# Kernel optimization log

Hardware: AMD Instinct MI355X
Metric: run time of the kernel (lower is better)

The kernel has to match this reference:

```python
import jax, jax.numpy as jnp
import numpy as np

D = 512; H = 8; HD = D // H; L = 6; QD = 16; MAXLEN = 1000

def _pos_encoding(max_len, d):
    pos = jnp.arange(max_len, dtype=jnp.float32)[:, None]
    div = jnp.exp(jnp.arange(0, d, 2, dtype=jnp.float32) * (-np.log(10000.0) / d))
    pe = jnp.zeros((max_len, d), jnp.float32)
    pe = pe.at[:, 0::2].set(jnp.sin(pos * div))
    pe = pe.at[:, 1::2].set(jnp.cos(pos * div))
    return pe

def _quantum(x, W, b, qwr, qwi, sg, em, mb):
    # QuantumInspiredLayer: classical tanh branch + quantum branch fused by sigmoid gate
    classical = jnp.tanh(x @ W + b)
    qs = x @ sg                          # (B,S,QD) real superposition amplitudes
    ev_r = qs @ qwr                      # complex evolution, real/imag parts kept separate
    ev_i = qs @ qwi
    en_r = ev_r @ em                     # entanglement (real matrix)
    en_i = ev_i @ em
    probs = en_r ** 2 + en_i ** 2        # |entangled|^2, (B,S,QD)
    qout = probs @ mb                    # measurement, (B,S,D)
    fw = jax.nn.sigmoid(jnp.mean(probs, axis=-1, keepdims=True))  # (B,S,1)
    return fw * qout + (1.0 - fw) * classical, probs

def _layer(x, p):
    (Wq, bq, Wk, bk, Wv, bv, Wo, bo,
     qW, qb, qr, qi, qsg, qem, qmb,
     kW, kb, kr, ki, ksg, kem, kmb, g, beta) = p
    B, S, _ = x.shape
    Q = x @ Wq + bq
    K = x @ Wk + bk
    Vv = x @ Wv + bv
    Qq, qp = _quantum(x, qW, qb, qr, qi, qsg, qem, qmb)
    Kq, kp = _quantum(x, kW, kb, kr, ki, ksg, kem, kmb)
    Qf = (0.7 * Q + 0.3 * Qq).reshape(B, S, H, HD).transpose(0, 2, 1, 3)  # (B,H,S,hd)
    Kf = (0.7 * K + 0.3 * Kq).reshape(B, S, H, HD).transpose(0, 2, 1, 3)
    Vh = Vv.reshape(B, S, H, HD).transpose(0, 2, 1, 3)
    scores = jnp.einsum('bhid,bhjd->bhij', Qf, Kf) / np.sqrt(HD).astype(np.float32)
    interf = jnp.einsum('biq,bjq->bij', qp, kp)   # quantum interference term (B,S,S)
    scores = scores + 0.1 * interf[:, None]       # broadcast over heads
    attn = jax.nn.softmax(scores, axis=-1)        # dropout=eval mode (identity)
    ctx = jnp.einsum('bhij,bhjd->bhid', attn, Vh).transpose(0, 2, 1, 3).reshape(B, S, D)
    y = ctx @ Wo + bo + x                         # residual, then LayerNorm
    mu = jnp.mean(y, axis=-1, keepdims=True)
    var = jnp.mean((y - mu) ** 2, axis=-1, keepdims=True)
    y = (y - mu) / jnp.sqrt(var + 1e-5) * g + beta
    return y, attn

def setup_inputs() -> dict:
    key = jax.random.key(0)
    ks = iter(jax.random.split(key, 64))
    def rn(shape, s=0.02):
        return (jax.random.normal(next(ks), shape) * s).astype(jnp.float32)
    B, S, V = 4, 512, 32000
    inp = {
        'text_input': jax.random.randint(next(ks), (B, S), 0, V),
        'visual_input': rn((B, 2048), 1.0),
        'temporal_input': rn((B, 64), 1.0),
        'embed': rn((V, D)),
        'Wvis': rn((2048, D)), 'bvis': jnp.zeros((D,), jnp.float32),
        'Wtemp': rn((64, D)), 'btemp': jnp.zeros((D,), jnp.float32),
        'Wq': rn((L, D, D)), 'bq': jnp.zeros((L, D), jnp.float32),
        'Wk': rn((L, D, D)), 'bk': jnp.zeros((L, D), jnp.float32),
        'Wv': rn((L, D, D)), 'bv': jnp.zeros((L, D), jnp.float32),
        'Wo': rn((L, D, D)), 'bo': jnp.zeros((L, D), jnp.float32),
        'qW': rn((L, D, D)), 'qb': jnp.zeros((L, D), jnp.float32),
        'q_qwr': rn((L, QD, QD), 0.05), 'q_qwi': rn((L, QD, QD), 0.05),
        'q_sg': rn((L, D, QD), 0.05), 'q_em': rn((L, QD, QD), 0.05), 'q_mb': rn((L, QD, D), 0.05),
        'kW': rn((L, D, D)), 'kb': jnp.zeros((L, D), jnp.float32),
        'k_qwr': rn((L, QD, QD), 0.05), 'k_qwi': rn((L, QD, QD), 0.05),
        'k_sg': rn((L, D, QD), 0.05), 'k_em': rn((L, QD, QD), 0.05), 'k_mb': rn((L, QD, D), 0.05),
        'ln_g': jnp.ones((L, D), jnp.float32), 'ln_b': jnp.zeros((L, D), jnp.float32),
        'Ws': rn((D, 64)), 'bs_': jnp.zeros((64,), jnp.float32),
        'Wd': rn((D, 5)), 'bd': jnp.zeros((5,), jnp.float32),
        'We': rn((D, 1)), 'be': jnp.zeros((1,), jnp.float32),
    }
    return inp

def reference(text_input, visual_input, temporal_input, embed, Wvis, bvis, Wtemp, btemp,
              Wq, bq, Wk, bk, Wv, bv, Wo, bo,
              qW, qb, q_qwr, q_qwi, q_sg, q_em, q_mb,
              kW, kb, k_qwr, k_qwi, k_sg, k_em, k_mb,
              ln_g, ln_b, Ws, bs_, Wd, bd, We, be):
    B, S = text_input.shape
    x = (embed[text_input]
         + (visual_input @ Wvis + bvis)[:, None, :]
         + (temporal_input @ Wtemp + btemp)[:, None, :])
    x = x + _pos_encoding(MAXLEN, D)[None, :S, :]
    attns = []
    for l in range(L):
        p = (Wq[l], bq[l], Wk[l], bk[l], Wv[l], bv[l], Wo[l], bo[l],
             qW[l], qb[l], q_qwr[l], q_qwi[l], q_sg[l], q_em[l], q_mb[l],
             kW[l], kb[l], k_qwr[l], k_qwi[l], k_sg[l], k_em[l], k_mb[l],
             ln_g[l], ln_b[l])
        x, a = _layer(x, p)
        attns.append(a)
    pooled = jnp.mean(x, axis=1)  # no attention_mask -> simple mean pool
    skill = jax.nn.sigmoid(pooled @ Ws + bs_)
    diff = jax.nn.softmax(pooled @ Wd + bd, axis=-1)
    eng = jax.nn.sigmoid(pooled @ We + be)
    return skill, diff, eng, x, jnp.stack(attns)
```

## Files before the change

### kernel.cpp

```cpp
#include <hip/hip_runtime.h>
#include <hip/hip_bf16.h>

typedef __attribute__((ext_vector_type(4))) float f32x4;
typedef __attribute__((ext_vector_type(8))) short s16x8;

__device__ __forceinline__ unsigned short f2b(float f) {
  unsigned int u = __float_as_uint(f);
  unsigned int r = (u + 0x7FFFu + ((u >> 16) & 1u)) >> 16;
  return (unsigned short)r;
}
__device__ __forceinline__ float b2f(unsigned short h) {
  return __uint_as_float(((unsigned int)h) << 16);
}
__device__ __forceinline__ void gload16(const void* g, void* l) {
  __builtin_amdgcn_global_load_lds(
      (const __attribute__((address_space(1))) void*)g,
      (__attribute__((address_space(3))) void*)l, 16, 0, 0);
}

enum { MODE_F32 = 0, MODE_VT = 1, MODE_Y = 2 };
struct OutSpec { void* ptr; int mode; };
struct Outs5 { OutSpec o[5]; };
struct Ptr6 { const float* p[6]; };

template<int BM, int BN, int WGM, int WGN>
__global__ __launch_bounds__(256) void gemm_nt(
    const unsigned short* __restrict__ A, int lda, long long strideA,
    const unsigned short* __restrict__ Bm, int ldb, long long strideB,
    const float* __restrict__ biasBase, int biasStride, int perZ,
    Outs5 outs, const float* __restrict__ resid, int K)
{
  constexpr int BK = 32;
  constexpr int WM = BM / WGM, WN = BN / WGN;
  constexpr int WR = WM / 16, WC = WN / 16;
  constexpr int CHA = BM * BK / 8;
  constexpr int CHB = BN * BK / 8;
  __shared__ unsigned short lds_a[2][BM * BK];
  __shared__ unsigned short lds_b[2][BN * BK];
  const int z = blockIdx.z;
  const int tid = threadIdx.x;
  const int wave = tid >> 6, lane = tid & 63;
  const int l16 = lane & 15, lhi = lane >> 4;
  const int wm = (wave / WGN) * WM, wn = (wave % WGN) * WN;
  const int m0 = blockIdx.x * BM, n0 = blockIdx.y * BN;
  const unsigned short* Ap = A + (long long)z * strideA;
  const unsigned short* Bp = Bm + (long long)z * strideB;

  auto stage = [&](int buf, int k0) {
#pragma unroll
    for (int p = 0; p < CHA / 256; ++p) {
      int t = p * 256 + tid;
      gload16(Ap + (long long)(m0 + (t >> 2)) * lda + k0 + (t & 3) * 8, &lds_a[buf][t * 8]);
    }
    if constexpr (CHA % 256) {
      if (tid < CHA % 256) {
        int t = (CHA / 256) * 256 + tid;
        gload16(Ap + (long long)(m0 + (t >> 2)) * lda + k0 + (t & 3) * 8, &lds_a[buf][t * 8]);
      }
    }
#pragma unroll
    for (int p = 0; p < CHB / 256; ++p) {
      int t = p * 256 + tid;
      gload16(Bp + (long long)(n0 + (t >> 2)) * ldb + k0 + (t & 3) * 8, &lds_b[buf][t * 8]);
    }
    if constexpr (CHB % 256) {
      if (tid < CHB % 256) {
        int t = (CHB / 256) * 256 + tid;
        gload16(Bp + (long long)(n0 + (t >> 2)) * ldb + k0 + (t & 3) * 8, &lds_b[buf][t * 8]);
      }
    }
  };

  f32x4 acc[WR][WC];
#pragma unroll
  for (int r = 0; r < WR; ++r)
#pragma unroll
    for (int c = 0; c < WC; ++c) { f32x4 zz = {0.f, 0.f, 0.f, 0.f}; acc[r][c] = zz; }

  stage(0, 0);
  __syncthreads();
  int cur = 0;
  for (int k0 = 0; k0 < K; k0 += BK) {
    if (k0 + BK < K) stage(cur ^ 1, k0 + BK);
    s16x8 af[WR], bfv[WC];
#pragma unroll
    for (int r = 0; r < WR; ++r)
      af[r] = *(const s16x8*)&lds_a[cur][(wm + r * 16 + l16) * BK + lhi * 8];
#pragma unroll
    for (int c = 0; c < WC; ++c)
      bfv[c] = *(const s16x8*)&lds_b[cur][(wn + c * 16 + l16) * BK + lhi * 8];
#pragma unroll
    for (int r = 0; r < WR; ++r)
#pragma unroll
      for (int c = 0; c < WC; ++c)
        acc[r][c] = __builtin_amdgcn_mfma_f32_16x16x32_bf16(af[r], bfv[c], acc[r][c], 0, 0, 0);
    __syncthreads();
    cur ^= 1;
  }

  OutSpec spec = perZ ? outs.o[z] : outs.o[0];
  const float* bias = biasBase ? (biasBase + (long long)z * biasStride) : nullptr;
#pragma unroll
  for (int r = 0; r < WR; ++r) {
#pragma unroll
    for (int c = 0; c < WC; ++c) {
      int n = n0 + wn + c * 16 + l16;
      int rb = m0 + wm + r * 16 + lhi * 4;
      float bv = bias ? bias[n] : 0.f;
      float vv[4];
#pragma unroll
      for (int j = 0; j < 4; ++j) vv[j] = acc[r][c][j] + bv;
      if (spec.mode == MODE_F32) {
#pragma unroll
        for (int j = 0; j < 4; ++j)
          ((float*)spec.ptr)[(long long)(rb + j) * 512 + n] = vv[j];
      } else if (spec.mode == MODE_VT) {
        int b = rb >> 9, s = rb & 511;
        ushort4 pk;
        pk.x = f2b(vv[0]); pk.y = f2b(vv[1]); pk.z = f2b(vv[2]); pk.w = f2b(vv[3]);
        *(ushort4*)&((unsigned short*)spec.ptr)[
            (((long long)(b * 8 + (n >> 6))) * 64 + (n & 63)) * 512 + s] = pk;
      } else {
#pragma unroll
        for (int j = 0; j < 4; ++j)
          ((float*)spec.ptr)[(long long)(rb + j) * 512 + n] =
              vv[j] + resid[(long long)(rb + j) * 512 + n];
      }
    }
  }
}

__global__ __launch_bounds__(256, 1) void fused_attn(
    const unsigned short* __restrict__ Qe, const unsigned short* __restrict__ Ke,
    const unsigned short* __restrict__ Vt, float* __restrict__ attn,
    unsigned short* __restrict__ ctx)
{
  __shared__ unsigned short lds[55296];
  const int z = blockIdx.x, rb = blockIdx.y;
  const int m0 = rb * 64;
  const int b = z >> 3, h = z & 7;
  const int tid = threadIdx.x;
  const int w = tid >> 6, lane = tid & 63;
  const int l16 = lane & 15, lhi = lane >> 4;
  const int rx3 = l16 & 3, rx7 = l16 & 7;

#pragma unroll
  for (int p = 0; p < 3; ++p) {
    int t = p * 256 + tid;
    int row = t / 12, c = t % 12;
    gload16(Qe + ((long long)(z * 512 + m0 + row)) * 96 + (c ^ (row & 3)) * 8, &lds[t * 8]);
  }
#pragma unroll
  for (int p = 0; p < 24; ++p) {
    int t = p * 256 + tid;
    int row = t / 12, c = t % 12;
    gload16(Ke + ((long long)(z * 512 + row)) * 96 + (c ^ (row & 3)) * 8, &lds[6144 + t * 8]);
  }
  __syncthreads();

  const unsigned short* Qs = lds;
  const unsigned short* Ks = lds + 6144;
  s16x8 aq[3];
#pragma unroll
  for (int kk = 0; kk < 3; ++kk)
    aq[kk] = *(const s16x8*)&Qs[(w * 16 + l16) * 96 + (kk * 4 + (lhi ^ rx3)) * 8];
  f32x4 acc[32];
#pragma unroll
  for (int c = 0; c < 32; ++c) { f32x4 zz = {0.f, 0.f, 0.f, 0.f}; acc[c] = zz; }
#pragma unroll
  for (int c = 0; c < 32; ++c) {
#pragma unroll
    for (int kk = 0; kk < 3; ++kk) {
      s16x8 bf = *(const s16x8*)&Ks[(c * 16 + l16) * 96 + (kk * 4 + (lhi ^ rx3)) * 8];
      acc[c] = __builtin_amdgcn_mfma_f32_16x16x32_bf16(aq[kk], bf, acc[c], 0, 0, 0);
    }
  }

  float inv[4];
#pragma unroll
  for (int j = 0; j < 4; ++j) {
    float mx = acc[0][j];
#pragma unroll
    for (int c = 1; c < 32; ++c) mx = fmaxf(mx, acc[c][j]);
    mx = fmaxf(mx, __shfl_xor(mx, 1));
    mx = fmaxf(mx, __shfl_xor(mx, 2));
    mx = fmaxf(mx, __shfl_xor(mx, 4));
    mx = fmaxf(mx, __shfl_xor(mx, 8));
    float sum = 0.f;
#pragma unroll
    for (int c = 0; c < 32; ++c) { float e = __expf(acc[c][j] - mx); acc[c][j] = e; sum += e; }
    sum += __shfl_xor(sum, 1);
    sum += __shfl_xor(sum, 2);
    sum += __shfl_xor(sum, 4);
    sum += __shfl_xor(sum, 8);
    inv[j] = 1.f / sum;
  }
  __syncthreads();

#pragma unroll
  for (int p = 0; p < 8; ++p) {
    int t = p * 256 + tid;
    int row = t >> 5, c = t & 31;
    gload16(Vt + (long long)z * 32768 + row * 512 + (c ^ (row & 7)) * 8, &lds[32768 + t * 8]);
  }
  unsigned short* S = lds;
  {
    float* ap = attn + (long long)z * 262144;
#pragma unroll
    for (int j = 0; j < 4; ++j) {
      int row_l = w * 16 + lhi * 4 + j;
      int rs = row_l & 7;
      float* arow = ap + (long long)(m0 + row_l) * 512;
      unsigned short* srow = S + row_l * 512;
#pragma unroll
      for (int c = 0; c < 32; ++c) {
        float p = acc[c][j] * inv[j];
        int col = c * 16 + l16;
        arow[col] = p;
        srow[((col >> 3) ^ rs) * 8 + (col & 7)] = f2b(p);
      }
    }
  }
  __syncthreads();

  const unsigned short* Vl = lds + 32768;
  f32x4 acc2[4];
#pragma unroll
  for (int c2 = 0; c2 < 4; ++c2) { f32x4 zz = {0.f, 0.f, 0.f, 0.f}; acc2[c2] = zz; }
  const int qrow = w * 16 + l16;
#pragma unroll
  for (int kk = 0; kk < 8; ++kk) {
    s16x8 a = *(const s16x8*)&S[qrow * 512 + ((kk * 4 + lhi) ^ rx7) * 8];
#pragma unroll
    for (int c2 = 0; c2 < 4; ++c2) {
      s16x8 bf = *(const s16x8*)&Vl[(c2 * 16 + l16) * 256 + ((kk * 4 + lhi) ^ rx7) * 8];
      acc2[c2] = __builtin_amdgcn_mfma_f32_16x16x32_bf16(a, bf, acc2[c2], 0, 0, 0);
    }
  }
  __syncthreads();
#pragma unroll
  for (int p = 0; p < 8; ++p) {
    int t = p * 256 + tid;
    int row = t >> 5, c = t & 31;
    gload16(Vt + (long long)z * 32768 + row * 512 + 256 + (c ^ (row & 7)) * 8,
            &lds[32768 + t * 8]);
  }
  __syncthreads();
#pragma unroll
  for (int kk = 8; kk < 16; ++kk) {
    s16x8 a = *(const s16x8*)&S[qrow * 512 + ((kk * 4 + lhi) ^ rx7) * 8];
#pragma unroll
    for (int c2 = 0; c2 < 4; ++c2) {
      s16x8 bf = *(const s16x8*)&Vl[(c2 * 16 + l16) * 256 + (((kk - 8) * 4 + lhi) ^ rx7) * 8];
      acc2[c2] = __builtin_amdgcn_mfma_f32_16x16x32_bf16(a, bf, acc2[c2], 0, 0, 0);
    }
  }
#pragma unroll
  for (int c2 = 0; c2 < 4; ++c2) {
#pragma unroll
    for (int j = 0; j < 4; ++j) {
      int row_g = m0 + w * 16 + lhi * 4 + j;
      ctx[((long long)(b * 512 + row_g)) * 512 + h * 64 + c2 * 16 + l16] = f2b(acc2[c2][j]);
    }
  }
}

__global__ __launch_bounds__(256) void wt_k(Ptr6 srcs, unsigned short* __restrict__ wt) {
  __shared__ float tile[32][33];
  int zz = blockIdx.z;
  int l = zz / 6, mat = zz % 6;
  const float* src = srcs.p[mat] + (long long)l * 262144;
  int tx = threadIdx.x, ty = threadIdx.y;
  int n0 = blockIdx.x * 32, k0 = blockIdx.y * 32;
#pragma unroll
  for (int r = 0; r < 4; ++r)
    tile[ty + r * 8][tx] = src[(long long)(k0 + ty + r * 8) * 512 + n0 + tx];
  __syncthreads();
#pragma unroll
  for (int r = 0; r < 4; ++r)
    wt[(long long)zz * 262144 + (long long)(n0 + ty + r * 8) * 512 + k0 + tx] =
        f2b(tile[tx][ty + r * 8]);
}

__global__ __launch_bounds__(256) void prep_k(Ptr6 biases,
    const float* __restrict__ qwr, const float* __restrict__ qwi, const float* __restrict__ qem,
    const float* __restrict__ kwr, const float* __restrict__ kwi, const float* __restrict__ kem,
    float* __restrict__ biasPacked, float* __restrict__ ArAi) {
  int l = blockIdx.x, t = threadIdx.x;
  for (int m = 0; m < 6; ++m)
    for (int d = t; d < 512; d += 256)
      biasPacked[(l * 6 + m) * 512 + d] = biases.p[m][l * 512 + d];
  int i = t >> 4, j = t & 15;
  const float* em0 = qem + l * 256;
  float ar = 0.f, ai = 0.f;
  for (int tt = 0; tt < 16; ++tt) {
    ar += qwr[l * 256 + i * 16 + tt] * em0[tt * 16 + j];
    ai += qwi[l * 256 + i * 16 + tt] * em0[tt * 16 + j];
  }
  ArAi[(l * 4 + 0) * 256 + t] = ar;
  ArAi[(l * 4 + 1) * 256 + t] = ai;
  const float* em1 = kem + l * 256;
  ar = 0.f; ai = 0.f;
  for (int tt = 0; tt < 16; ++tt) {
    ar += kwr[l * 256 + i * 16 + tt] * em1[tt * 16 + j];
    ai += kwi[l * 256 + i * 16 + tt] * em1[tt * 16 + j];
  }
  ArAi[(l * 4 + 2) * 256 + t] = ar;
  ArAi[(l * 4 + 3) * 256 + t] = ai;
}

__global__ __launch_bounds__(512) void vispart_k(const float* __restrict__ vis,
    const float* __restrict__ Wvis, float* __restrict__ part) {
  int b = blockIdx.x, chunk = blockIdx.y, d = threadIdx.x;
  float acc = 0.f;
  for (int k = chunk * 64; k < chunk * 64 + 64; ++k)
    acc += vis[b * 2048 + k] * Wvis[(long long)k * 512 + d];
  part[(b * 32 + chunk) * 512 + d] = acc;
}
__global__ __launch_bounds__(512) void projsum_k(const float* __restrict__ part,
    const float* __restrict__ bvis, const float* __restrict__ temporal,
    const float* __restrict__ Wtemp, const float* __restrict__ btemp, float* __restrict__ proj) {
  int b = blockIdx.x, d = threadIdx.x;
  float acc = bvis[d] + btemp[d];
  for (int c = 0; c < 32; ++c) acc += part[(b * 32 + c) * 512 + d];
  for (int k = 0; k < 64; ++k) acc += temporal[b * 64 + k] * Wtemp[k * 512 + d];
  proj[b * 512 + d] = acc;
}

__global__ __launch_bounds__(512) void embed_k(const int* __restrict__ text,
    const float* __restrict__ emb, const float* __restrict__ proj,
    float* __restrict__ x, unsigned short* __restrict__ xb) {
  int row = blockIdx.x;
  int b = row >> 9, s = row & 511;
  int d = threadIdx.x;
  int tok = text[row];
  float v = emb[(long long)tok * 512 + d] + proj[b * 512 + d];
  float fr = __expf((float)((d >> 1) << 1) * (-9.2103403719761836f / 512.f));
  float ang = (float)s * fr;
  v += (d & 1) ? cosf(ang) : sinf(ang);
  x[(long long)row * 512 + d] = v;
  xb[(long long)row * 512 + d] = f2b(v);
}

__global__ __launch_bounds__(64) void quantum_k(const float* __restrict__ x,
    const float* __restrict__ sg_q, const float* __restrict__ sg_k,
    const float* __restrict__ ArAiL, float* __restrict__ qp, float* __restrict__ kp,
    float* __restrict__ fwq, float* __restrict__ fwk) {
  int row = blockIdx.x, side = blockIdx.y, lane = threadIdx.x;
  const float* sg = side ? sg_k : sg_q;
  const float* Ar = ArAiL + side * 512;
  const float* Ai = Ar + 256;
  float acc[16];
#pragma unroll
  for (int j = 0; j < 16; ++j) acc[j] = 0.f;
  const float* xr = x + (long long)row * 512;
#pragma unroll
  for (int kk = 0; kk < 8; ++kk) {
    float xv = xr[kk * 64 + lane];
    const float* sgr = sg + (kk * 64 + lane) * 16;
#pragma unroll
    for (int j = 0; j < 16; ++j) acc[j] += xv * sgr[j];
  }
#pragma unroll
  for (int s = 32; s; s >>= 1)
#pragma unroll
    for (int j = 0; j < 16; ++j) acc[j] += __shfl_xor(acc[j], s);
  int j = lane & 15;
  float tr = 0.f, ti = 0.f;
#pragma unroll
  for (int t = 0; t < 16; ++t) {
    tr += acc[t] * Ar[t * 16 + j];
    ti += acc[t] * Ai[t * 16 + j];
  }
  float p = tr * tr + ti * ti;
  float ps = p;
#pragma unroll
  for (int s = 1; s < 16; s <<= 1) ps += __shfl_xor(ps, s);
  if (lane < 16) (side ? kp : qp)[row * 16 + lane] = p;
  if (lane == 0) (side ? fwk : fwq)[row] = 1.f / (1.f + __expf(-ps * (1.f / 16.f)));
}

struct FuseP {
  const float* lin; const float* cl; const float* qp; const float* fw;
  const float* mb; unsigned short* ext; float sA, sB;
};
struct Fuse2 { FuseP s[2]; };
__global__ __launch_bounds__(512) void fuse_k(Fuse2 fp) {
  FuseP P = fp.s[blockIdx.y];
  int row = blockIdx.x;
  int b = row >> 9, i = row & 511;
  int d = threadIdx.x;
  const float* qpr = P.qp + row * 16;
  float fwv = P.fw[row];
  float qout = 0.f;
#pragma unroll
  for (int t = 0; t < 16; ++t) qout += qpr[t] * P.mb[t * 512 + d];
  float qq = fwv * qout + (1.f - fwv) * tanhf(P.cl[(long long)row * 512 + d]);
  float val = (0.7f * P.lin[(long long)row * 512 + d] + 0.3f * qq) * P.sA;
  int h = d >> 6, dd = d & 63;
  P.ext[(((long long)(b * 8 + h)) * 512 + i) * 96 + dd] = f2b(val);
  if (d < 128) {
    int h2 = d >> 4, j = d & 15;
    P.ext[(((long long)(b * 8 + h2)) * 512 + i) * 96 + 64 + j] = f2b(P.sB * qpr[j]);
  } else if (d < 256) {
    int t2 = d - 128;
    int h2 = t2 >> 4, j = t2 & 15;
    P.ext[(((long long)(b * 8 + h2)) * 512 + i) * 96 + 80 + j] = 0;
  }
}

__global__ __launch_bounds__(256) void ln_k(const float* __restrict__ y,
    const float* __restrict__ g, const float* __restrict__ be,
    float* __restrict__ xo, unsigned short* __restrict__ xb, float* __restrict__ xo2) {
  int wv = threadIdx.x >> 6, lane = threadIdx.x & 63;
  long long row = (long long)blockIdx.x * 4 + wv;
  const float* yr = y + row * 512 + lane * 8;
  f32x4 a = *(const f32x4*)yr, b = *(const f32x4*)(yr + 4);
  float s = a[0] + a[1] + a[2] + a[3] + b[0] + b[1] + b[2] + b[3];
#pragma unroll
  for (int m = 32; m; m >>= 1) s += __shfl_xor(s, m);
  float mu = s * (1.f / 512.f);
  float d[8], vs = 0.f;
#pragma unroll
  for (int j = 0; j < 4; ++j) { d[j] = a[j] - mu; vs += d[j] * d[j]; }
#pragma unroll
  for (int j = 0; j < 4; ++j) { d[4 + j] = b[j] - mu; vs += d[4 + j] * d[4 + j]; }
#pragma unroll
  for (int m = 32; m; m >>= 1) vs += __shfl_xor(vs, m);
  float rstd = rsqrtf(vs * (1.f / 512.f) + 1e-5f);
  f32x4 g0 = *(const f32x4*)(g + lane * 8), g1 = *(const f32x4*)(g + lane * 8 + 4);
  f32x4 b0 = *(const f32x4*)(be + lane * 8), b1 = *(const f32x4*)(be + lane * 8 + 4);
  f32x4 o0, o1; s16x8 ob;
#pragma unroll
  for (int j = 0; j < 4; ++j) { o0[j] = d[j] * rstd * g0[j] + b0[j]; ob[j] = (short)f2b(o0[j]); }
#pragma unroll
  for (int j = 0; j < 4; ++j) { o1[j] = d[4 + j] * rstd * g1[j] + b1[j]; ob[4 + j] = (short)f2b(o1[j]); }
  float* xr = xo + row * 512 + lane * 8;
  *(f32x4*)xr = o0; *(f32x4*)(xr + 4) = o1;
  *(s16x8*)(xb + row * 512 + lane * 8) = ob;
  if (xo2) {
    float* x2 = xo2 + row * 512 + lane * 8;
    *(f32x4*)x2 = o0; *(f32x4*)(x2 + 4) = o1;
  }
}

__global__ __launch_bounds__(512) void poolpart_k(const float* __restrict__ x,
                                                   float* __restrict__ part) {
  int b = blockIdx.x, ch = blockIdx.y, d = threadIdx.x;
  float s = 0.f;
  for (int r = 0; r < 64; ++r) s += x[((long long)(b * 512 + ch * 64 + r)) * 512 + d];
  part[(b * 8 + ch) * 512 + d] = s;
}
__global__ __launch_bounds__(512) void head_k(const float* __restrict__ part,
    const float* __restrict__ Ws, const float* __restrict__ bs,
    const float* __restrict__ Wd, const float* __restrict__ bd,
    const float* __restrict__ We, const float* __restrict__ be, float* __restrict__ out) {
  __shared__ float pooled[512];
  __shared__ float dl[5];
  int b = blockIdx.x, d = threadIdx.x;
  float s = 0.f;
  for (int t = 0; t < 8; ++t) s += part[(b * 8 + t) * 512 + d];
  pooled[d] = s * (1.f / 512.f);
  __syncthreads();
  if (d < 64) {
    float a = bs[d];
    for (int t = 0; t < 512; ++t) a += pooled[t] * Ws[t * 64 + d];
    out[b * 64 + d] = 1.f / (1.f + __expf(-a));
  } else if (d < 69) {
    int j = d - 64;
    float a = bd[j];
    for (int t = 0; t < 512; ++t) a += pooled[t] * Wd[t * 5 + j];
    dl[j] = a;
  } else if (d == 69) {
    float a = be[0];
    for (int t = 0; t < 512; ++t) a += pooled[t] * We[t];
    out[276 + b] = 1.f / (1.f + __expf(-a));
  }
  __syncthreads();
  if (d < 5) {
    float mx = dl[0];
    for (int j = 1; j < 5; ++j) mx = fmaxf(mx, dl[j]);
    float sm = 0.f;
    for (int j = 0; j < 5; ++j) sm += __expf(dl[j] - mx);
    out[256 + b * 5 + d] = __expf(dl[d] - mx) / sm;
  }
}

extern "C" void kernel_launch(void* const* d_in, const int* in_sizes, int n_in,
                              void* d_out, int out_size, void* d_ws, size_t ws_size,
                              hipStream_t stream) {
  (void)in_sizes; (void)n_in; (void)out_size; (void)ws_size;
  const int*   text     = (const int*)  d_in[0];
  const float* visual   = (const float*)d_in[1];
  const float* temporal = (const float*)d_in[2];
  const float* embedw   = (const float*)d_in[3];
  const float* Wvis  = (const float*)d_in[4];  const float* bvis  = (const float*)d_in[5];
  const float* Wtemp = (const float*)d_in[6];  const float* btemp = (const float*)d_in[7];
  const float* Wq = (const float*)d_in[8];   const float* bq = (const float*)d_in[9];
  const float* Wk = (const float*)d_in[10];  const float* bk = (const float*)d_in[11];
  const float* Wv = (const float*)d_in[12];  const float* bv = (const float*)d_in[13];
  const float* Wo = (const float*)d_in[14];  const float* bo = (const float*)d_in[15];
  const float* qW = (const float*)d_in[16];  const float* qb = (const float*)d_in[17];
  const float* q_qwr = (const float*)d_in[18]; const float* q_qwi = (const float*)d_in[19];
  const float* q_sg  = (const float*)d_in[20]; const float* q_em  = (const float*)d_in[21];
  const float* q_mb  = (const float*)d_in[22];
  const float* kW = (const float*)d_in[23];  const float* kb = (const float*)d_in[24];
  const float* k_qwr = (const float*)d_in[25]; const float* k_qwi = (const float*)d_in[26];
  const float* k_sg  = (const float*)d_in[27]; const float* k_em  = (const float*)d_in[28];
  const float* k_mb  = (const float*)d_in[29];
  const float* ln_g = (const float*)d_in[30]; const float* ln_b = (const float*)d_in[31];
  const float* Ws = (const float*)d_in[32];  const float* bs_ = (const float*)d_in[33];
  const float* Wd = (const float*)d_in[34];  const float* bd = (const float*)d_in[35];
  const float* We = (const float*)d_in[36];  const float* be = (const float*)d_in[37];
  float* out = (float*)d_out;

  char* w = (char*)d_ws;
  auto alloc = [&](size_t bytes) {
    char* p = w;
    w += (bytes + 255) & ~(size_t)255;
    return p;
  };
  float* ws_x   = (float*)alloc(2048ll * 512 * 4);
  unsigned short* ws_xb = (unsigned short*)alloc(2048ll * 512 * 2);
  unsigned short* ws_Wt = (unsigned short*)alloc(36ll * 262144 * 2);
  float* ws_bias = (float*)alloc(6ll * 6 * 512 * 4);
  float* ws_ArAi = (float*)alloc(6ll * 1024 * 4);
  float* ws_proj = (float*)alloc(4ll * 512 * 4);
  float* ws_vp   = (float*)alloc(4ll * 32 * 512 * 4);
  float* ws_Q    = (float*)alloc(2048ll * 512 * 4);
  float* ws_K    = (float*)alloc(2048ll * 512 * 4);
  float* ws_Cq   = (float*)alloc(2048ll * 512 * 4);
  float* ws_Ck   = (float*)alloc(2048ll * 512 * 4);
  float* ws_qp   = (float*)alloc(2048ll * 16 * 4);
  float* ws_kp   = (float*)alloc(2048ll * 16 * 4);
  float* ws_fwq  = (float*)alloc(2048ll * 4);
  float* ws_fwk  = (float*)alloc(2048ll * 4);
  unsigned short* ws_Vt   = (unsigned short*)alloc(2048ll * 512 * 2);
  unsigned short* ws_Qext = (unsigned short*)alloc(4ll * 8 * 512 * 96 * 2);
  unsigned short* ws_Kext = (unsigned short*)alloc(4ll * 8 * 512 * 96 * 2);
  unsigned short* ws_ctx  = (unsigned short*)alloc(2048ll * 512 * 2);
  float* ws_y    = (float*)alloc(2048ll * 512 * 4);

  Ptr6 wsrc = {{Wq, Wk, Wv, qW, kW, Wo}};
  wt_k<<<dim3(16, 16, 36), dim3(32, 8), 0, stream>>>(wsrc, ws_Wt);
  Ptr6 bsrc = {{bq, bk, bv, qb, kb, bo}};
  prep_k<<<dim3(6), dim3(256), 0, stream>>>(bsrc, q_qwr, q_qwi, q_em, k_qwr, k_qwi, k_em,
                                            ws_bias, ws_ArAi);
  vispart_k<<<dim3(4, 32), dim3(512), 0, stream>>>(visual, Wvis, ws_vp);
  projsum_k<<<dim3(4), dim3(512), 0, stream>>>(ws_vp, bvis, temporal, Wtemp, btemp, ws_proj);
  embed_k<<<dim3(2048), dim3(512), 0, stream>>>(text, embedw, ws_proj, ws_x, ws_xb);

  const long long ATTN_OFF = 280ll + 1048576ll;
  for (int l = 0; l < 6; ++l) {
    const unsigned short* WtL = ws_Wt + (long long)l * 6 * 262144;
    const float* biasL = ws_bias + (long long)l * 6 * 512;

    Outs5 o5{};
    o5.o[0] = { ws_Q, MODE_F32 };  o5.o[1] = { ws_K, MODE_F32 };
    o5.o[2] = { ws_Vt, MODE_VT };  o5.o[3] = { ws_Cq, MODE_F32 };
    o5.o[4] = { ws_Ck, MODE_F32 };
    gemm_nt<128, 128, 2, 2><<<dim3(16, 4, 5), 256, 0, stream>>>(
        ws_xb, 512, 0ll, WtL, 512, 262144ll, biasL, 512, 1, o5, nullptr, 512);

    quantum_k<<<dim3(2048, 2), 64, 0, stream>>>(ws_x, q_sg + l * 8192, k_sg + l * 8192,
        ws_ArAi + l * 1024, ws_qp, ws_kp, ws_fwq, ws_fwk);

    Fuse2 f2{};
    f2.s[0] = { ws_Q, ws_Cq, ws_qp, ws_fwq, q_mb + l * 8192, ws_Qext, 0.125f, 0.1f };
    f2.s[1] = { ws_K, ws_Ck, ws_kp, ws_fwk, k_mb + l * 8192, ws_Kext, 1.0f, 1.0f };
    fuse_k<<<dim3(2048, 2), dim3(512), 0, stream>>>(f2);

    fused_attn<<<dim3(32, 8), 256, 0, stream>>>(
        ws_Qext, ws_Kext, ws_Vt, out + ATTN_OFF + (long long)l * 8388608, ws_ctx);

    Outs5 oy{};
    oy.o[0] = { ws_y, MODE_Y };
    gemm_nt<64, 64, 2, 2><<<dim3(32, 8, 1), 256, 0, stream>>>(
        ws_ctx, 512, 0ll, WtL + 5 * 262144, 512, 0ll, biasL + 5 * 512, 0, 0, oy, ws_x, 512);

    ln_k<<<dim3(512), dim3(256), 0, stream>>>(ws_y, ln_g + l * 512, ln_b + l * 512,
        ws_x, ws_xb, (l == 5) ? (out + 280) : nullptr);
  }

  poolpart_k<<<dim3(4, 8), dim3(512), 0, stream>>>(ws_x, ws_vp);
  head_k<<<dim3(4), dim3(512), 0, stream>>>(ws_vp, Ws, bs_, Wd, bd, We, be, out);
}
```

Before: 507.8 us.

## Store GEMM intermediates in bf16 and prefetch K/V earlier in attention

The projection and Wo GEMM outputs (Q, K, classical branches and the pre-LayerNorm sum) are now stored as bf16 instead of fp32, and fuse_k and ln_k read bf16. This halves their memory traffic. quantum_k now reads the bf16 copy of x instead of the fp32 one. In fused_attn, K is loaded in two halves and the first V half is prefetched up front into a larger LDS buffer, with partial vmcnt waits and s_setprio so the QK^T MFMAs overlap the loads. In exchange, bf16 rounding of the residual sum before LayerNorm and of the quantum input may reduce accuracy, and the larger LDS footprint limits occupancy.

```diff
diff --git a/kernel.cpp b/kernel.cpp
--- a/kernel.cpp
+++ b/kernel.cpp
@@ -18,7 +18,7 @@
       (__attribute__((address_space(3))) void*)l, 16, 0, 0);
 }
 
-enum { MODE_F32 = 0, MODE_VT = 1, MODE_Y = 2 };
+enum { MODE_BF16 = 0, MODE_VT = 1, MODE_Y = 2 };
 struct OutSpec { void* ptr; int mode; };
 struct Outs5 { OutSpec o[5]; };
 struct Ptr6 { const float* p[6]; };
@@ -110,10 +110,10 @@
       float vv[4];
 #pragma unroll
       for (int j = 0; j < 4; ++j) vv[j] = acc[r][c][j] + bv;
-      if (spec.mode == MODE_F32) {
+      if (spec.mode == MODE_BF16) {
 #pragma unroll
         for (int j = 0; j < 4; ++j)
-          ((float*)spec.ptr)[(long long)(rb + j) * 512 + n] = vv[j];
+          ((unsigned short*)spec.ptr)[(long long)(rb + j) * 512 + n] = f2b(vv[j]);
       } else if (spec.mode == MODE_VT) {
         int b = rb >> 9, s = rb & 511;
         ushort4 pk;
@@ -123,8 +123,8 @@
       } else {
 #pragma unroll
         for (int j = 0; j < 4; ++j)
-          ((float*)spec.ptr)[(long long)(rb + j) * 512 + n] =
-              vv[j] + resid[(long long)(rb + j) * 512 + n];
+          ((unsigned short*)spec.ptr)[(long long)(rb + j) * 512 + n] =
+              f2b(vv[j] + resid[(long long)(rb + j) * 512 + n]);
       }
     }
   }
@@ -135,46 +135,73 @@
     const unsigned short* __restrict__ Vt, float* __restrict__ attn,
     unsigned short* __restrict__ ctx)
 {
-  __shared__ unsigned short lds[55296];
+  __shared__ unsigned short lds[71680];
   const int z = blockIdx.x, rb = blockIdx.y;
-  const int m0 = rb * 64;
-  const int b = z >> 3, h = z & 7;
-  const int tid = threadIdx.x;
-  const int w = tid >> 6, lane = tid & 63;
+  const int m0 = rb * 64, b = z >> 3, h = z & 7;
+  const int tid = threadIdx.x, w = tid >> 6, lane = tid & 63;
   const int l16 = lane & 15, lhi = lane >> 4;
   const int rx3 = l16 & 3, rx7 = l16 & 7;
+  const long long zs = (long long)z * 512;
 
 #pragma unroll
   for (int p = 0; p < 3; ++p) {
     int t = p * 256 + tid;
     int row = t / 12, c = t % 12;
-    gload16(Qe + ((long long)(z * 512 + m0 + row)) * 96 + (c ^ (row & 3)) * 8, &lds[t * 8]);
-  }
-#pragma unroll
-  for (int p = 0; p < 24; ++p) {
+    gload16(Qe + (zs + m0 + row) * 96 + (c ^ (row & 3)) * 8, &lds[t * 8]);
+  }
+#pragma unroll
+  for (int p = 0; p < 12; ++p) {
     int t = p * 256 + tid;
     int row = t / 12, c = t % 12;
-    gload16(Ke + ((long long)(z * 512 + row)) * 96 + (c ^ (row & 3)) * 8, &lds[6144 + t * 8]);
-  }
-  __syncthreads();
-
-  const unsigned short* Qs = lds;
-  const unsigned short* Ks = lds + 6144;
+    gload16(Ke + (zs + row) * 96 + (c ^ (row & 3)) * 8, &lds[6144 + t * 8]);
+  }
+#pragma unroll
+  for (int p = 0; p < 12; ++p) {
+    int t = p * 256 + tid;
+    int row = t / 12, c = t % 12;
+    gload16(Ke + (zs + 256 + row) * 96 + (c ^ (row & 3)) * 8, &lds[30720 + t * 8]);
+  }
+#pragma unroll
+  for (int p = 0; p < 8; ++p) {
+    int t = p * 256 + tid;
+    int row = t >> 5, c = t & 31;
+    gload16(Vt + (long long)z * 32768 + row * 512 + (c ^ (row & 7)) * 8, &lds[55296 + t * 8]);
+  }
+  asm volatile("s_waitcnt vmcnt(20)" ::: "memory");
+  __builtin_amdgcn_s_barrier();
+  __builtin_amdgcn_sched_barrier(0);
+
   s16x8 aq[3];
 #pragma unroll
   for (int kk = 0; kk < 3; ++kk)
-    aq[kk] = *(const s16x8*)&Qs[(w * 16 + l16) * 96 + (kk * 4 + (lhi ^ rx3)) * 8];
+    aq[kk] = *(const s16x8*)&lds[(w * 16 + l16) * 96 + (kk * 4 + (lhi ^ rx3)) * 8];
   f32x4 acc[32];
 #pragma unroll
   for (int c = 0; c < 32; ++c) { f32x4 zz = {0.f, 0.f, 0.f, 0.f}; acc[c] = zz; }
-#pragma unroll
-  for (int c = 0; c < 32; ++c) {
+  __builtin_amdgcn_s_setprio(1);
+#pragma unroll
+  for (int c = 0; c < 16; ++c)
 #pragma unroll
     for (int kk = 0; kk < 3; ++kk) {
-      s16x8 bf = *(const s16x8*)&Ks[(c * 16 + l16) * 96 + (kk * 4 + (lhi ^ rx3)) * 8];
+      s16x8 bf = *(const s16x8*)&lds[6144 + (c * 16 + l16) * 96 + (kk * 4 + (lhi ^ rx3)) * 8];
       acc[c] = __builtin_amdgcn_mfma_f32_16x16x32_bf16(aq[kk], bf, acc[c], 0, 0, 0);
     }
-  }
+  __builtin_amdgcn_s_setprio(0);
+  asm volatile("s_waitcnt vmcnt(8)" ::: "memory");
+  __builtin_amdgcn_s_barrier();
+  __builtin_amdgcn_sched_barrier(0);
+
+  __builtin_amdgcn_s_setprio(1);
+#pragma unroll
+  for (int c = 16; c < 32; ++c)
+#pragma unroll
+    for (int kk = 0; kk < 3; ++kk) {
+      s16x8 bf = *(const s16x8*)&lds[30720 + ((c - 16) * 16 + l16) * 96 + (kk * 4 + (lhi ^ rx3)) * 8];
+      acc[c] = __builtin_amdgcn_mfma_f32_16x16x32_bf16(aq[kk], bf, acc[c], 0, 0, 0);
+    }
+  __builtin_amdgcn_s_setprio(0);
+  __builtin_amdgcn_s_barrier();
+  __builtin_amdgcn_sched_barrier(0);
 
   float inv[4];
 #pragma unroll
@@ -195,14 +222,7 @@
     sum += __shfl_xor(sum, 8);
     inv[j] = 1.f / sum;
   }
-  __syncthreads();
-
-#pragma unroll
-  for (int p = 0; p < 8; ++p) {
-    int t = p * 256 + tid;
-    int row = t >> 5, c = t & 31;
-    gload16(Vt + (long long)z * 32768 + row * 512 + (c ^ (row & 7)) * 8, &lds[32768 + t * 8]);
-  }
+
   unsigned short* S = lds;
   {
     float* ap = attn + (long long)z * 262144;
@@ -223,21 +243,6 @@
   }
   __syncthreads();
 
-  const unsigned short* Vl = lds + 32768;
-  f32x4 acc2[4];
-#pragma unroll
-  for (int c2 = 0; c2 < 4; ++c2) { f32x4 zz = {0.f, 0.f, 0.f, 0.f}; acc2[c2] = zz; }
-  const int qrow = w * 16 + l16;
-#pragma unroll
-  for (int kk = 0; kk < 8; ++kk) {
-    s16x8 a = *(const s16x8*)&S[qrow * 512 + ((kk * 4 + lhi) ^ rx7) * 8];
-#pragma unroll
-    for (int c2 = 0; c2 < 4; ++c2) {
-      s16x8 bf = *(const s16x8*)&Vl[(c2 * 16 + l16) * 256 + ((kk * 4 + lhi) ^ rx7) * 8];
-      acc2[c2] = __builtin_amdgcn_mfma_f32_16x16x32_bf16(a, bf, acc2[c2], 0, 0, 0);
-    }
-  }
-  __syncthreads();
 #pragma unroll
   for (int p = 0; p < 8; ++p) {
     int t = p * 256 + tid;
@@ -245,16 +250,35 @@
     gload16(Vt + (long long)z * 32768 + row * 512 + 256 + (c ^ (row & 7)) * 8,
             &lds[32768 + t * 8]);
   }
+  f32x4 acc2[4];
+#pragma unroll
+  for (int c2 = 0; c2 < 4; ++c2) { f32x4 zz = {0.f, 0.f, 0.f, 0.f}; acc2[c2] = zz; }
+  const int qrow = w * 16 + l16;
+  __builtin_amdgcn_s_setprio(1);
+#pragma unroll
+  for (int kk = 0; kk < 8; ++kk) {
+    s16x8 a = *(const s16x8*)&S[qrow * 512 + ((kk * 4 + lhi) ^ rx7) * 8];
+#pragma unroll
+    for (int c2 = 0; c2 < 4; ++c2) {
+      s16x8 bf = *(const s16x8*)&lds[55296 + (c2 * 16 + l16) * 256 + ((kk * 4 + lhi) ^ rx7) * 8];
+      acc2[c2] = __builtin_amdgcn_mfma_f32_16x16x32_bf16(a, bf, acc2[c2], 0, 0, 0);
+    }
+  }
+  __builtin_amdgcn_s_setprio(0);
   __syncthreads();
+
+  __builtin_amdgcn_s_setprio(1);
 #pragma unroll
   for (int kk = 8; kk < 16; ++kk) {
     s16x8 a = *(const s16x8*)&S[qrow * 512 + ((kk * 4 + lhi) ^ rx7) * 8];
 #pragma unroll
     for (int c2 = 0; c2 < 4; ++c2) {
-      s16x8 bf = *(const s16x8*)&Vl[(c2 * 16 + l16) * 256 + (((kk - 8) * 4 + lhi) ^ rx7) * 8];
+      s16x8 bf = *(const s16x8*)&lds[32768 + (c2 * 16 + l16) * 256 + (((kk - 8) * 4 + lhi) ^ rx7) * 8];
       acc2[c2] = __builtin_amdgcn_mfma_f32_16x16x32_bf16(a, bf, acc2[c2], 0, 0, 0);
     }
   }
+  __builtin_amdgcn_s_setprio(0);
+
 #pragma unroll
   for (int c2 = 0; c2 < 4; ++c2) {
 #pragma unroll
@@ -342,7 +366,7 @@
   xb[(long long)row * 512 + d] = f2b(v);
 }
 
-__global__ __launch_bounds__(64) void quantum_k(const float* __restrict__ x,
+__global__ __launch_bounds__(64) void quantum_k(const unsigned short* __restrict__ xb,
     const float* __restrict__ sg_q, const float* __restrict__ sg_k,
     const float* __restrict__ ArAiL, float* __restrict__ qp, float* __restrict__ kp,
     float* __restrict__ fwq, float* __restrict__ fwk) {
@@ -353,11 +377,11 @@
   float acc[16];
 #pragma unroll
   for (int j = 0; j < 16; ++j) acc[j] = 0.f;
-  const float* xr = x + (long long)row * 512;
-#pragma unroll
-  for (int kk = 0; kk < 8; ++kk) {
-    float xv = xr[kk * 64 + lane];
-    const float* sgr = sg + (kk * 64 + lane) * 16;
+  s16x8 xv8 = *(const s16x8*)(xb + (long long)row * 512 + lane * 8);
+#pragma unroll
+  for (int e = 0; e < 8; ++e) {
+    float xv = b2f((unsigned short)xv8[e]);
+    const float* sgr = sg + (lane * 8 + e) * 16;
 #pragma unroll
     for (int j = 0; j < 16; ++j) acc[j] += xv * sgr[j];
   }
@@ -381,7 +405,7 @@
 }
 
 struct FuseP {
-  const float* lin; const float* cl; const float* qp; const float* fw;
+  const unsigned short* lin; const unsigned short* cl; const float* qp; const float* fw;
   const float* mb; unsigned short* ext; float sA, sB;
 };
 struct Fuse2 { FuseP s[2]; };
@@ -395,8 +419,8 @@
   float qout = 0.f;
 #pragma unroll
   for (int t = 0; t < 16; ++t) qout += qpr[t] * P.mb[t * 512 + d];
-  float qq = fwv * qout + (1.f - fwv) * tanhf(P.cl[(long long)row * 512 + d]);
-  float val = (0.7f * P.lin[(long long)row * 512 + d] + 0.3f * qq) * P.sA;
+  float qq = fwv * qout + (1.f - fwv) * tanhf(b2f(P.cl[(long long)row * 512 + d]));
+  float val = (0.7f * b2f(P.lin[(long long)row * 512 + d]) + 0.3f * qq) * P.sA;
   int h = d >> 6, dd = d & 63;
   P.ext[(((long long)(b * 8 + h)) * 512 + i) * 96 + dd] = f2b(val);
   if (d < 128) {
@@ -409,22 +433,21 @@
   }
 }
 
-__global__ __launch_bounds__(256) void ln_k(const float* __restrict__ y,
+__global__ __launch_bounds__(256) void ln_k(const unsigned short* __restrict__ y,
     const float* __restrict__ g, const float* __restrict__ be,
     float* __restrict__ xo, unsigned short* __restrict__ xb, float* __restrict__ xo2) {
   int wv = threadIdx.x >> 6, lane = threadIdx.x & 63;
   long long row = (long long)blockIdx.x * 4 + wv;
-  const float* yr = y + row * 512 + lane * 8;
-  f32x4 a = *(const f32x4*)yr, b = *(const f32x4*)(yr + 4);
-  float s = a[0] + a[1] + a[2] + a[3] + b[0] + b[1] + b[2] + b[3];
+  s16x8 yv = *(const s16x8*)(y + row * 512 + lane * 8);
+  float f[8], s = 0.f;
+#pragma unroll
+  for (int j = 0; j < 8; ++j) { f[j] = b2f((unsigned short)yv[j]); s += f[j]; }
 #pragma unroll
   for (int m = 32; m; m >>= 1) s += __shfl_xor(s, m);
   float mu = s * (1.f / 512.f);
   float d[8], vs = 0.f;
 #pragma unroll
-  for (int j = 0; j < 4; ++j) { d[j] = a[j] - mu; vs += d[j] * d[j]; }
-#pragma unroll
-  for (int j = 0; j < 4; ++j) { d[4 + j] = b[j] - mu; vs += d[4 + j] * d[4 + j]; }
+  for (int j = 0; j < 8; ++j) { d[j] = f[j] - mu; vs += d[j] * d[j]; }
 #pragma unroll
   for (int m = 32; m; m >>= 1) vs += __shfl_xor(vs, m);
   float rstd = rsqrtf(vs * (1.f / 512.f) + 1e-5f);
@@ -527,10 +550,10 @@
   float* ws_ArAi = (float*)alloc(6ll * 1024 * 4);
   float* ws_proj = (float*)alloc(4ll * 512 * 4);
   float* ws_vp   = (float*)alloc(4ll * 32 * 512 * 4);
-  float* ws_Q    = (float*)alloc(2048ll * 512 * 4);
-  float* ws_K    = (float*)alloc(2048ll * 512 * 4);
-  float* ws_Cq   = (float*)alloc(2048ll * 512 * 4);
-  float* ws_Ck   = (float*)alloc(2048ll * 512 * 4);
+  unsigned short* ws_Q  = (unsigned short*)alloc(2048ll * 512 * 2);
+  unsigned short* ws_K  = (unsigned short*)alloc(2048ll * 512 * 2);
+  unsigned short* ws_Cq = (unsigned short*)alloc(2048ll * 512 * 2);
+  unsigned short* ws_Ck = (unsigned short*)alloc(2048ll * 512 * 2);
   float* ws_qp   = (float*)alloc(2048ll * 16 * 4);
   float* ws_kp   = (float*)alloc(2048ll * 16 * 4);
   float* ws_fwq  = (float*)alloc(2048ll * 4);
@@ -539,7 +562,7 @@
   unsigned short* ws_Qext = (unsigned short*)alloc(4ll * 8 * 512 * 96 * 2);
   unsigned short* ws_Kext = (unsigned short*)alloc(4ll * 8 * 512 * 96 * 2);
   unsigned short* ws_ctx  = (unsigned short*)alloc(2048ll * 512 * 2);
-  float* ws_y    = (float*)alloc(2048ll * 512 * 4);
+  unsigned short* ws_y    = (unsigned short*)alloc(2048ll * 512 * 2);
 
   Ptr6 wsrc = {{Wq, Wk, Wv, qW, kW, Wo}};
   wt_k<<<dim3(16, 16, 36), dim3(32, 8), 0, stream>>>(wsrc, ws_Wt);
@@ -556,13 +579,13 @@
     const float* biasL = ws_bias + (long long)l * 6 * 512;
 
     Outs5 o5{};
-    o5.o[0] = { ws_Q, MODE_F32 };  o5.o[1] = { ws_K, MODE_F32 };
-    o5.o[2] = { ws_Vt, MODE_VT };  o5.o[3] = { ws_Cq, MODE_F32 };
-    o5.o[4] = { ws_Ck, MODE_F32 };
+    o5.o[0] = { ws_Q, MODE_BF16 };  o5.o[1] = { ws_K, MODE_BF16 };
+    o5.o[2] = { ws_Vt, MODE_VT };   o5.o[3] = { ws_Cq, MODE_BF16 };
+    o5.o[4] = { ws_Ck, MODE_BF16 };
     gemm_nt<128, 128, 2, 2><<<dim3(16, 4, 5), 256, 0, stream>>>(
         ws_xb, 512, 0ll, WtL, 512, 262144ll, biasL, 512, 1, o5, nullptr, 512);
 
-    quantum_k<<<dim3(2048, 2), 64, 0, stream>>>(ws_x, q_sg + l * 8192, k_sg + l * 8192,
+    quantum_k<<<dim3(2048, 2), 64, 0, stream>>>(ws_xb, q_sg + l * 8192, k_sg + l * 8192,
         ws_ArAi + l * 1024, ws_qp, ws_kp, ws_fwq, ws_fwk);
 
     Fuse2 f2{};
```

Result: slower. 547.3 us (+7.8%).
